# Performance work log

Hardware: AMD Instinct MI355X
Metric: run time of the kernel (lower is better)

## Reference

```python
import jax, jax.numpy as jnp
import numpy as np

IN_UNITS = 128
N_DRUG, N_DIS, N_EDGE = 10000, 5000, 2000000


def setup_inputs() -> dict:
    key = jax.random.key(0)
    ks = jax.random.split(key, 10)
    s1 = 1.0 / np.sqrt(2 * IN_UNITS)
    s2 = 1.0 / np.sqrt(128)
    s3 = 1.0 / np.sqrt(64)
    return {
        "drug_feat": jax.random.normal(ks[0], (N_DRUG, IN_UNITS), dtype=jnp.float32),
        "dis_feat": jax.random.normal(ks[1], (N_DIS, IN_UNITS), dtype=jnp.float32),
        "edge_index": jax.random.randint(ks[2], (2, N_EDGE), 0, N_DIS, dtype=jnp.int64),
        "W1": jax.random.uniform(ks[3], (128, 2 * IN_UNITS), jnp.float32, -s1, s1),
        "b1": jax.random.uniform(ks[4], (128,), jnp.float32, -s1, s1),
        "W2": jax.random.uniform(ks[5], (64, 128), jnp.float32, -s2, s2),
        "b2": jax.random.uniform(ks[6], (64,), jnp.float32, -s2, s2),
        "W3": jax.random.uniform(ks[7], (1, 64), jnp.float32, -s3, s3),
        "b3": jax.random.uniform(ks[8], (1,), jnp.float32, -s3, s3),
    }


def reference(drug_feat, dis_feat, edge_index, W1, b1, W2, b2, W3, b3):
    # Gather endpoint features and concat along feature dim: [E, 2*in_units]
    edge_feat = jnp.concatenate(
        (drug_feat[edge_index[0]], dis_feat[edge_index[1]]), axis=1
    )
    # 3-layer MLP (Dropout is identity in eval mode)
    h = jax.nn.relu(edge_feat @ W1.T + b1)  # [E, 128]
    h = jax.nn.relu(h @ W2.T + b2)          # [E, 64]
    return h @ W3.T + b3                     # [E, 1]
```

## Files before the change

### kernel.cpp

```cpp
#include <hip/hip_runtime.h>


typedef __bf16 bf16x8 __attribute__((ext_vector_type(8)));
typedef unsigned short u16x8 __attribute__((ext_vector_type(8)));
typedef float f32x4 __attribute__((ext_vector_type(4)));

static __device__ __forceinline__ unsigned short f2b(float f) {
  unsigned int u = __builtin_bit_cast(unsigned int, f);
  u += 0x7FFFu + ((u >> 16) & 1u);
  return (unsigned short)(u >> 16);
}

static __device__ __forceinline__ f32x4 mfma_bf16(u16x8 a, u16x8 b, f32x4 c) {
  return __builtin_amdgcn_mfma_f32_16x16x32_bf16(
      __builtin_bit_cast(bf16x8, a), __builtin_bit_cast(bf16x8, b), c, 0, 0, 0);
}

__global__ void cvt_tables(const float* __restrict__ a, const float* __restrict__ b,
                           unsigned short* __restrict__ oa, unsigned short* __restrict__ ob,
                           int na, int nb) {
  const int t = blockIdx.x * blockDim.x + threadIdx.x;
  const int ta = na >> 3;
  const float* src;
  unsigned short* dst;
  int i;
  if (t < ta) {
    src = a; dst = oa; i = t;
  } else {
    i = t - ta;
    if (i >= (nb >> 3)) return;
    src = b; dst = ob;
  }
  const float4 f0 = *(const float4*)(src + i * 8);
  const float4 f1 = *(const float4*)(src + i * 8 + 4);
  u16x8 v;
  v[0] = f2b(f0.x); v[1] = f2b(f0.y); v[2] = f2b(f0.z); v[3] = f2b(f0.w);
  v[4] = f2b(f1.x); v[5] = f2b(f1.y); v[6] = f2b(f1.z); v[7] = f2b(f1.w);
  *(u16x8*)(dst + i * 8) = v;
}

__global__ void cvt_weights(const float* __restrict__ W1, const float* __restrict__ W2,
                            unsigned short* __restrict__ o1, unsigned short* __restrict__ o2) {
  const int t = blockIdx.x * blockDim.x + threadIdx.x;
  if (t < 4096) {
    const int l = t & 63, kt = (t >> 6) & 7, ut = t >> 9;
    const int n = 16 * ut + (l & 15), k0 = 32 * kt + 8 * (l >> 4);
    const float* src = W1 + n * 256 + k0;
    u16x8 v;
#pragma unroll
    for (int j = 0; j < 8; ++j) v[j] = f2b(src[j]);
    *(u16x8*)(o1 + t * 8) = v;
  } else if (t < 5120) {
    const int u = t - 4096;
    const int l = u & 63, kt = (u >> 6) & 3, nt = u >> 8;
    const int n = 16 * nt + (l & 15), k0 = 32 * kt + 8 * (l >> 4);
    const float* src = W2 + n * 128 + k0;
    u16x8 v;
#pragma unroll
    for (int j = 0; j < 8; ++j) v[j] = f2b(src[j]);
    *(u16x8*)(o2 + u * 8) = v;
  }
}

__global__ __launch_bounds__(256, 4) void mlp_fused(
    const unsigned short* __restrict__ drugB, const unsigned short* __restrict__ disB,
    const int* __restrict__ eidx, const unsigned short* __restrict__ w1frag,
    const unsigned short* __restrict__ w2frag, const float* __restrict__ b1,
    const float* __restrict__ b2, const float* __restrict__ W3,
    const float* __restrict__ b3, float* __restrict__ out, int E) {
  __shared__ __align__(16) unsigned char smem[33792];
  unsigned char* Abase = smem;
  float* partials = (float*)(smem + 32768);

  const int tid = threadIdx.x;
  const int wn = tid >> 6;
  const int l = tid & 63;
  const int l15 = l & 15;
  const int lq = l >> 4;
  const int e0 = blockIdx.x * 64;

  const int aoff = lq * 1024 + l15 * 16;

  {
    int e = e0 + l;
    if (e >= E) e = E - 1;
    const int idx = eidx[(wn >> 1) * E + e];
    const unsigned short* src = ((wn < 2) ? drugB : disB) + (long)idx * 128 + (wn & 1) * 64;
    unsigned char* wbase = Abase + wn * 8192 + l * 16;
#pragma unroll
    for (int c = 0; c < 8; ++c) {
      const u16x8 v = *(const u16x8*)(src + c * 8);
      *(u16x8*)(wbase + c * 1024) = v;
    }
  }

  u16x8 w2f[4];
#pragma unroll
  for (int kt = 0; kt < 4; ++kt)
    w2f[kt] = *(const u16x8*)(w2frag + ((wn * 4 + kt) * 64 + l) * 8);
  const float4 b1v0 = *(const float4*)(b1 + 32 * wn + 4 * lq);
  const float4 b1v1 = *(const float4*)(b1 + 32 * wn + 16 + 4 * lq);
  const float4 b2v = *(const float4*)(b2 + 16 * wn + 4 * lq);
  const float4 w3v = *(const float4*)(W3 + 16 * wn + 4 * lq);
  __syncthreads();

  f32x4 acc1[2][4];
#pragma unroll
  for (int uti = 0; uti < 2; ++uti)
#pragma unroll
    for (int nt = 0; nt < 4; ++nt) acc1[uti][nt] = (f32x4){0.f, 0.f, 0.f, 0.f};

  const unsigned short* w1p = w1frag + ((2 * wn) * 512 + l) * 8;
  u16x8 nf[2][2];
  nf[0][0] = *(const u16x8*)(w1p);
  nf[0][1] = *(const u16x8*)(w1p + 512 * 8);
  nf[1][0] = *(const u16x8*)(w1p + 64 * 8);
  nf[1][1] = *(const u16x8*)(w1p + (512 + 64) * 8);
#pragma unroll
  for (int kt = 0; kt < 8; ++kt) {
    const u16x8 c0 = nf[kt & 1][0], c1 = nf[kt & 1][1];
    if (kt < 6) {
      nf[kt & 1][0] = *(const u16x8*)(w1p + ((kt + 2) * 64) * 8);
      nf[kt & 1][1] = *(const u16x8*)(w1p + ((512 + (kt + 2) * 64)) * 8);
    }
#pragma unroll
    for (int nt = 0; nt < 4; ++nt) {
      const u16x8 b = *(const u16x8*)(Abase + kt * 4096 + nt * 256 + aoff);
      acc1[0][nt] = mfma_bf16(c0, b, acc1[0][nt]);
      acc1[1][nt] = mfma_bf16(c1, b, acc1[1][nt]);
    }
  }
  __syncthreads();

  {
    unsigned char* hw = Abase + wn * 4096 + (lq >> 1) * 1024 + (lq & 1) * 8 + l15 * 16;
#pragma unroll
    for (int uti = 0; uti < 2; ++uti) {
      const float4 bv = uti ? b1v1 : b1v0;
#pragma unroll
      for (int nt = 0; nt < 4; ++nt) {
        float h0 = acc1[uti][nt][0] + bv.x; h0 = h0 > 0.f ? h0 : 0.f;
        float h1 = acc1[uti][nt][1] + bv.y; h1 = h1 > 0.f ? h1 : 0.f;
        float h2 = acc1[uti][nt][2] + bv.z; h2 = h2 > 0.f ? h2 : 0.f;
        float h3 = acc1[uti][nt][3] + bv.w; h3 = h3 > 0.f ? h3 : 0.f;
        ushort4 hv;
        hv.x = f2b(h0); hv.y = f2b(h1); hv.z = f2b(h2); hv.w = f2b(h3);
        *(ushort4*)(hw + uti * 2048 + nt * 256) = hv;
      }
    }
  }
  __syncthreads();

  f32x4 acc2[4];
#pragma unroll
  for (int nt = 0; nt < 4; ++nt) acc2[nt] = (f32x4){0.f, 0.f, 0.f, 0.f};
#pragma unroll
  for (int kt = 0; kt < 4; ++kt) {
#pragma unroll
    for (int nt = 0; nt < 4; ++nt) {
      const u16x8 b = *(const u16x8*)(Abase + kt * 4096 + nt * 256 + aoff);
      acc2[nt] = mfma_bf16(w2f[kt], b, acc2[nt]);
    }
  }

#pragma unroll
  for (int nt = 0; nt < 4; ++nt) {
    float h0 = acc2[nt][0] + b2v.x; h0 = h0 > 0.f ? h0 : 0.f;
    float h1 = acc2[nt][1] + b2v.y; h1 = h1 > 0.f ? h1 : 0.f;
    float h2 = acc2[nt][2] + b2v.z; h2 = h2 > 0.f ? h2 : 0.f;
    float h3 = acc2[nt][3] + b2v.w; h3 = h3 > 0.f ? h3 : 0.f;
    float s = h0 * w3v.x + h1 * w3v.y + h2 * w3v.z + h3 * w3v.w;
    s += __shfl_xor(s, 16, 64);
    s += __shfl_xor(s, 32, 64);
    if (l < 16) partials[wn * 64 + 16 * nt + l15] = s;
  }
  __syncthreads();

  if (tid < 64) {
    const int e = e0 + tid;
    if (e < E) {
      out[e] = partials[tid] + partials[64 + tid] + partials[128 + tid] +
               partials[192 + tid] + b3[0];
    }
  }
}

extern "C" void kernel_launch(void* const* d_in, const int* in_sizes, int n_in,
                              void* d_out, int out_size, void* d_ws, size_t ws_size,
                              hipStream_t stream) {
  const float* drug = (const float*)d_in[0];
  const float* dis = (const float*)d_in[1];
  const int* eidx = (const int*)d_in[2];
  const float* W1 = (const float*)d_in[3];
  const float* b1 = (const float*)d_in[4];
  const float* W2 = (const float*)d_in[5];
  const float* b2 = (const float*)d_in[6];
  const float* W3 = (const float*)d_in[7];
  const float* b3 = (const float*)d_in[8];
  float* out = (float*)d_out;

  const int na = in_sizes[0];
  const int nb = in_sizes[1];
  const int E = in_sizes[2] / 2;

  unsigned short* ws = (unsigned short*)d_ws;
  unsigned short* drugB = ws;
  unsigned short* disB = ws + na;
  unsigned short* w1f = ws + na + nb;
  unsigned short* w2f = w1f + 128 * 256;

  const int tct = (na + nb) >> 3;
  cvt_tables<<<(tct + 255) / 256, 256, 0, stream>>>(drug, dis, drugB, disB, na, nb);
  cvt_weights<<<20, 256, 0, stream>>>(W1, W2, w1f, w2f);

  const int grid = (E + 63) / 64;
  mlp_fused<<<grid, 256, 0, stream>>>(drugB, disB, eidx, w1f, w2f, b1, b2, W3, b3, out, E);
}
```

Before: 224.0 us.

## Switch layer-1 GEMM to 32x32x16 MFMA with reworked weight fragment layout

Layer 1 now uses 32x32x16 bf16 MFMA tiles instead of 16x16x32. Each wave computes 64 output units across 32 edges, with a 4-deep register prefetch of W1 fragments. The W1 fragment packing and the LDS layout for the hidden activations are changed to match. The goal is fewer MFMA issues and fewer LDS B-fragment reads per wave. In exchange it uses larger accumulators and has a different LDS bank access pattern.

Result: slower. 287.1 us (+28.1%).

```diff
diff --git a/kernel.cpp b/kernel.cpp
--- a/kernel.cpp
+++ b/kernel.cpp
@@ -4,6 +4,7 @@
 typedef __bf16 bf16x8 __attribute__((ext_vector_type(8)));
 typedef unsigned short u16x8 __attribute__((ext_vector_type(8)));
 typedef float f32x4 __attribute__((ext_vector_type(4)));
+typedef float f32x16 __attribute__((ext_vector_type(16)));
 
 static __device__ __forceinline__ unsigned short f2b(float f) {
   unsigned int u = __builtin_bit_cast(unsigned int, f);
@@ -11,8 +12,12 @@
   return (unsigned short)(u >> 16);
 }
 
-static __device__ __forceinline__ f32x4 mfma_bf16(u16x8 a, u16x8 b, f32x4 c) {
+static __device__ __forceinline__ f32x4 mfma16(u16x8 a, u16x8 b, f32x4 c) {
   return __builtin_amdgcn_mfma_f32_16x16x32_bf16(
+      __builtin_bit_cast(bf16x8, a), __builtin_bit_cast(bf16x8, b), c, 0, 0, 0);
+}
+static __device__ __forceinline__ f32x16 mfma32(u16x8 a, u16x8 b, f32x16 c) {
+  return __builtin_amdgcn_mfma_f32_32x32x16_bf16(
       __builtin_bit_cast(bf16x8, a), __builtin_bit_cast(bf16x8, b), c, 0, 0, 0);
 }
 
@@ -43,8 +48,8 @@
                             unsigned short* __restrict__ o1, unsigned short* __restrict__ o2) {
   const int t = blockIdx.x * blockDim.x + threadIdx.x;
   if (t < 4096) {
-    const int l = t & 63, kt = (t >> 6) & 7, ut = t >> 9;
-    const int n = 16 * ut + (l & 15), k0 = 32 * kt + 8 * (l >> 4);
+    const int l = t & 63, s = (t >> 6) & 15, ut = t >> 10;
+    const int n = 32 * ut + (l & 31), k0 = 16 * s + 8 * (l >> 5);
     const float* src = W1 + n * 256 + k0;
     u16x8 v;
 #pragma unroll
@@ -73,20 +78,22 @@
   float* partials = (float*)(smem + 32768);
 
   const int tid = threadIdx.x;
-  const int wn = tid >> 6;
+  const int w = tid >> 6;
+  const int wn = w;
+  const int wn2 = w >> 1;
+  const int wm = w & 1;
   const int l = tid & 63;
   const int l15 = l & 15;
   const int lq = l >> 4;
+  const int hi = l >> 5;
   const int e0 = blockIdx.x * 64;
-
-  const int aoff = lq * 1024 + l15 * 16;
 
   {
     int e = e0 + l;
     if (e >= E) e = E - 1;
-    const int idx = eidx[(wn >> 1) * E + e];
-    const unsigned short* src = ((wn < 2) ? drugB : disB) + (long)idx * 128 + (wn & 1) * 64;
-    unsigned char* wbase = Abase + wn * 8192 + l * 16;
+    const int idx = eidx[(w >> 1) * E + e];
+    const unsigned short* src = ((w < 2) ? drugB : disB) + (long)idx * 128 + (w & 1) * 64;
+    unsigned char* wbase = Abase + w * 8192 + l * 16;
 #pragma unroll
     for (int c = 0; c < 8; ++c) {
       const u16x8 v = *(const u16x8*)(src + c * 8);
@@ -98,68 +105,64 @@
 #pragma unroll
   for (int kt = 0; kt < 4; ++kt)
     w2f[kt] = *(const u16x8*)(w2frag + ((wn * 4 + kt) * 64 + l) * 8);
-  const float4 b1v0 = *(const float4*)(b1 + 32 * wn + 4 * lq);
-  const float4 b1v1 = *(const float4*)(b1 + 32 * wn + 16 + 4 * lq);
   const float4 b2v = *(const float4*)(b2 + 16 * wn + 4 * lq);
   const float4 w3v = *(const float4*)(W3 + 16 * wn + 4 * lq);
   __syncthreads();
 
-  f32x4 acc1[2][4];
-#pragma unroll
-  for (int uti = 0; uti < 2; ++uti)
-#pragma unroll
-    for (int nt = 0; nt < 4; ++nt) acc1[uti][nt] = (f32x4){0.f, 0.f, 0.f, 0.f};
-
-  const unsigned short* w1p = w1frag + ((2 * wn) * 512 + l) * 8;
-  u16x8 nf[2][2];
-  nf[0][0] = *(const u16x8*)(w1p);
-  nf[0][1] = *(const u16x8*)(w1p + 512 * 8);
-  nf[1][0] = *(const u16x8*)(w1p + 64 * 8);
-  nf[1][1] = *(const u16x8*)(w1p + (512 + 64) * 8);
-#pragma unroll
-  for (int kt = 0; kt < 8; ++kt) {
-    const u16x8 c0 = nf[kt & 1][0], c1 = nf[kt & 1][1];
-    if (kt < 6) {
-      nf[kt & 1][0] = *(const u16x8*)(w1p + ((kt + 2) * 64) * 8);
-      nf[kt & 1][1] = *(const u16x8*)(w1p + ((512 + (kt + 2) * 64)) * 8);
-    }
+  f32x16 acc[2];
+#pragma unroll
+  for (int i = 0; i < 16; ++i) { acc[0][i] = 0.f; acc[1][i] = 0.f; }
+
+  const int boff = hi * 1024 + (32 * wm + (l & 31)) * 16;
+  const unsigned short* w1p = w1frag + ((2 * wn2) * 1024 + l) * 8;
+  u16x8 nf[4][2];
+#pragma unroll
+  for (int s = 0; s < 4; ++s) {
+    nf[s][0] = *(const u16x8*)(w1p + (s * 64) * 8);
+    nf[s][1] = *(const u16x8*)(w1p + (1024 + s * 64) * 8);
+  }
+#pragma unroll
+  for (int s = 0; s < 16; ++s) {
+    const u16x8 c0 = nf[s & 3][0], c1 = nf[s & 3][1];
+    if (s < 12) {
+      nf[s & 3][0] = *(const u16x8*)(w1p + ((s + 4) * 64) * 8);
+      nf[s & 3][1] = *(const u16x8*)(w1p + ((1024 + (s + 4) * 64)) * 8);
+    }
+    const u16x8 b = *(const u16x8*)(Abase + s * 2048 + boff);
+    acc[0] = mfma32(c0, b, acc[0]);
+    acc[1] = mfma32(c1, b, acc[1]);
+  }
+  __syncthreads();
+
+  {
+    const int ebyte = (32 * wm + (l & 31)) * 16;
+#pragma unroll
+    for (int uti = 0; uti < 2; ++uti) {
+#pragma unroll
+      for (int p = 0; p < 4; ++p) {
+        const float4 bv = *(const float4*)(b1 + 32 * (2 * wn2 + uti) + 8 * p + 4 * hi);
+        float h0 = acc[uti][4 * p + 0] + bv.x; h0 = h0 > 0.f ? h0 : 0.f;
+        float h1 = acc[uti][4 * p + 1] + bv.y; h1 = h1 > 0.f ? h1 : 0.f;
+        float h2 = acc[uti][4 * p + 2] + bv.z; h2 = h2 > 0.f ? h2 : 0.f;
+        float h3 = acc[uti][4 * p + 3] + bv.w; h3 = h3 > 0.f ? h3 : 0.f;
+        ushort4 hv;
+        hv.x = f2b(h0); hv.y = f2b(h1); hv.z = f2b(h2); hv.w = f2b(h3);
+        *(ushort4*)(Abase + (4 * (2 * wn2 + uti) + p) * 1024 + ebyte + 8 * hi) = hv;
+      }
+    }
+  }
+  __syncthreads();
+
+  const int aoff = lq * 1024 + l15 * 16;
+  f32x4 acc2[4];
+#pragma unroll
+  for (int nt = 0; nt < 4; ++nt) acc2[nt] = (f32x4){0.f, 0.f, 0.f, 0.f};
+#pragma unroll
+  for (int kt = 0; kt < 4; ++kt) {
 #pragma unroll
     for (int nt = 0; nt < 4; ++nt) {
       const u16x8 b = *(const u16x8*)(Abase + kt * 4096 + nt * 256 + aoff);
-      acc1[0][nt] = mfma_bf16(c0, b, acc1[0][nt]);
-      acc1[1][nt] = mfma_bf16(c1, b, acc1[1][nt]);
-    }
-  }
-  __syncthreads();
-
-  {
-    unsigned char* hw = Abase + wn * 4096 + (lq >> 1) * 1024 + (lq & 1) * 8 + l15 * 16;
-#pragma unroll
-    for (int uti = 0; uti < 2; ++uti) {
-      const float4 bv = uti ? b1v1 : b1v0;
-#pragma unroll
-      for (int nt = 0; nt < 4; ++nt) {
-        float h0 = acc1[uti][nt][0] + bv.x; h0 = h0 > 0.f ? h0 : 0.f;
-        float h1 = acc1[uti][nt][1] + bv.y; h1 = h1 > 0.f ? h1 : 0.f;
-        float h2 = acc1[uti][nt][2] + bv.z; h2 = h2 > 0.f ? h2 : 0.f;
-        float h3 = acc1[uti][nt][3] + bv.w; h3 = h3 > 0.f ? h3 : 0.f;
-        ushort4 hv;
-        hv.x = f2b(h0); hv.y = f2b(h1); hv.z = f2b(h2); hv.w = f2b(h3);
-        *(ushort4*)(hw + uti * 2048 + nt * 256) = hv;
-      }
-    }
-  }
-  __syncthreads();
-
-  f32x4 acc2[4];
-#pragma unroll
-  for (int nt = 0; nt < 4; ++nt) acc2[nt] = (f32x4){0.f, 0.f, 0.f, 0.f};
-#pragma unroll
-  for (int kt = 0; kt < 4; ++kt) {
-#pragma unroll
-    for (int nt = 0; nt < 4; ++nt) {
-      const u16x8 b = *(const u16x8*)(Abase + kt * 4096 + nt * 256 + aoff);
-      acc2[nt] = mfma_bf16(w2f[kt], b, acc2[nt]);
+      acc2[nt] = mfma16(w2f[kt], b, acc2[nt]);
     }
   }
 
```
